# Performance work log

Measured on AMD Instinct MI355X. Metric: run time of the kernel, lower is better.

Reference implementation:

```python
import jax, jax.numpy as jnp
import numpy as np

DROPOUT_RATE = 0.1  # reference runs deterministically (dropout disabled), matching eval-mode math


def setup_inputs() -> dict:
    key = jax.random.key(0)
    k1, k2, k3 = jax.random.split(key, 3)
    BH, S, D = 32, 2048, 64   # batch*heads, seq_len, d_head
    B = 2                      # true batch (mask batch dim)
    q = jax.random.normal(k1, (BH, S, D), dtype=jnp.float32)
    k = jax.random.normal(k2, (BH, S, D), dtype=jnp.float32)
    v = jax.random.normal(k3, (BH, S, D), dtype=jnp.float32)
    mask = jnp.zeros((B, S, S), dtype=jnp.float32)  # additive mask
    return {"q": q, "k": k, "v": v, "mask": mask}


def reference(q, k, v, mask):
    # Scaled dot-product attention with additive mask.
    # q,k,v: [BH, S, D]; mask: [B, S, S], tiled along batch to BH.
    dk = jnp.asarray(k.shape[-1], dtype=jnp.float32)
    scores = jnp.einsum('bqd,bkd->bqk', q, k) / jnp.sqrt(dk)  # [BH, S, S]
    reps = q.shape[0] // mask.shape[0]
    mask_t = jnp.tile(mask, (reps, 1, 1))                     # [BH, S, S]
    attn = jax.nn.softmax(scores + mask_t, axis=-1)
    out = jnp.einsum('bqk,bkd->bqd', attn, v)                 # [BH, S, D]
    # K.dropout omitted: deterministic reference (eval mode / identity)
    return out
```

## Files before the change

kernel.cpp:

```cpp
#include <hip/hip_runtime.h>


constexpr int cBH = 32;
constexpr int cS  = 2048;
constexpr int cD  = 64;
constexpr int cQT = 128;
constexpr int cNP = cS / 128;

typedef __bf16 bf16x8 __attribute__((ext_vector_type(8)));
typedef __bf16 bf16x4 __attribute__((ext_vector_type(4)));
typedef float  f32x4  __attribute__((ext_vector_type(4)));
typedef float  f32x16 __attribute__((ext_vector_type(16)));
typedef unsigned int u32x4 __attribute__((ext_vector_type(4)));

__device__ __forceinline__ unsigned short bfbits(float f) {
    return __builtin_bit_cast(unsigned short, (__bf16)f);
}
__device__ __forceinline__ bf16x4 pack4(f32x4 a) {
    bf16x4 r;
    r[0] = (__bf16)a[0]; r[1] = (__bf16)a[1];
    r[2] = (__bf16)a[2]; r[3] = (__bf16)a[3];
    return r;
}
__device__ __forceinline__ bf16x8 pack8s(f32x4 a, f32x4 b, float s) {
    bf16x8 r;
    r[0] = (__bf16)(a[0]*s); r[1] = (__bf16)(a[1]*s);
    r[2] = (__bf16)(a[2]*s); r[3] = (__bf16)(a[3]*s);
    r[4] = (__bf16)(b[0]*s); r[5] = (__bf16)(b[1]*s);
    r[6] = (__bf16)(b[2]*s); r[7] = (__bf16)(b[3]*s);
    return r;
}
__device__ __forceinline__ int gkey(int d) {
    return (d ^ (d >> 3)) & 7;
}

__global__ __launch_bounds__(256, 2)
void sdpa_flash_kernel(const float* __restrict__ q,
                       const float* __restrict__ k,
                       const float* __restrict__ v,
                       const float* __restrict__ mask,
                       float* __restrict__ out)
{
    __shared__ unsigned short sK[2][64 * 64];
    __shared__ unsigned short sV[2][64 * 64];

    const int tid  = threadIdx.x;
    const int wv   = tid >> 6;
    const int lane = tid & 63;
    const int l31  = lane & 31;
    const int h    = lane >> 5;
    const int swk  = (lane & 7) ^ (((lane >> 3) & 1) << 2);

    const int fid = blockIdx.x;
    const int bh  = (fid & 7) | ((fid >> 7) << 3);
    const int qb  = ((fid >> 3) & 15) * cQT;
    const int mb  = bh & 1;

    const float L2E = 1.4426950408889634f;

    bf16x8 aq[4];
    {
        const float* qp = q + ((size_t)bh * cS + qb + wv * 32 + l31) * cD + h * 8;
#pragma unroll
        for (int dc = 0; dc < 4; ++dc)
            aq[dc] = pack8s(*(const f32x4*)(qp + dc * 16),
                            *(const f32x4*)(qp + dc * 16 + 4), 0.125f * L2E);
    }

    f32x16 acc[2] = {};
    float lsum = 0.f;

    const int sr0 = tid >> 4;
    const int c4  = (tid & 15) << 2;
    const int ka0 = sr0 * 64
        + ((((c4 >> 3) ^ (sr0 & 7) ^ (((sr0 >> 3) & 1) << 2)) << 3))
        + (c4 & 7);
    const float* kg = k + (size_t)bh * cS * cD;
    const float* vg = v + (size_t)bh * cS * cD;
    const float* mq = mask + (size_t)mb * cS * cS
                           + (size_t)(qb + wv * 32 + l31) * cS + h * 4;

    const int g0 = gkey(l31);
    const int g1 = gkey(32 + l31);
    const int vb0 = l31 * 64;
    const int vb1 = (32 + l31) * 64;

#pragma unroll
    for (int t = 0; t < 2; ++t)
#pragma unroll
        for (int j = 0; j < 4; ++j) {
            f32x4 kj = *(const f32x4*)(kg + t * 4096 + j * 1024 + tid * 4);
            f32x4 vj = *(const f32x4*)(vg + t * 4096 + j * 1024 + tid * 4);
            *(bf16x4*)&sK[t][ka0 + j * 1024] = pack4(kj);
#pragma unroll
            for (int i = 0; i < 4; ++i) {
                int d = c4 + i;
                sV[t][d * 64 + ((((j * 2) + (sr0 >> 3)) ^ gkey(d)) << 3) + (sr0 & 7)]
                    = bfbits(vj[i]);
            }
        }

    for (int pt = 0; pt < cNP; ++pt) {
        const int base = pt * 2;
        const bool more = (pt + 1 < cNP);
        const int nb = more ? base + 2 : base;

        f32x4 KPe[4], VPe[4], KPo[4], VPo[4];
#pragma unroll
        for (int j = 0; j < 4; ++j) {
            KPe[j] = *(const f32x4*)(kg + (size_t)nb * 4096 + j * 1024 + tid * 4);
            VPe[j] = *(const f32x4*)(vg + (size_t)nb * 4096 + j * 1024 + tid * 4);
            KPo[j] = *(const f32x4*)(kg + (size_t)(nb + 1) * 4096 + j * 1024 + tid * 4);
            VPo[j] = *(const f32x4*)(vg + (size_t)(nb + 1) * 4096 + j * 1024 + tid * 4);
        }

        __syncthreads();

#pragma unroll
        for (int t = 0; t < 2; ++t) {
            const unsigned short* sKt = sK[t];
            const unsigned short* sVt = sV[t];
#pragma unroll
            for (int gg = 0; gg < 2; ++gg) {
                const float* mrow = mq + (size_t)(base + t) * 64 + gg * 32;
                f32x4 mk[4];
#pragma unroll
                for (int j = 0; j < 4; ++j)
                    mk[j] = *(const f32x4*)(mrow + j * 8);

                const int rb = (gg * 32 + l31) * 64;
                bf16x8 kf[4];
#pragma unroll
                for (int dc = 0; dc < 4; ++dc)
                    kf[dc] = *(const bf16x8*)(&sKt[rb + (((dc * 2 + h) ^ swk) << 3)]);
                f32x16 s = {};
#pragma unroll
                for (int dc = 0; dc < 4; ++dc)
                    s = __builtin_amdgcn_mfma_f32_32x32x16_bf16(kf[dc], aq[dc], s, 0, 0, 0);

                float p[16];
#pragma unroll
                for (int r = 0; r < 16; ++r)
                    p[r] = __builtin_amdgcn_exp2f(fmaf(mk[r >> 2][r & 3], L2E, s[r]));
#pragma unroll
                for (int r = 0; r < 16; ++r)
                    lsum += p[r];

                unsigned int pk[8];
#pragma unroll
                for (int i = 0; i < 8; ++i)
                    pk[i] = (unsigned int)bfbits(p[2 * i])
                          | ((unsigned int)bfbits(p[2 * i + 1]) << 16);
                asm("v_permlane32_swap_b32 %0, %1" : "+v"(pk[0]), "+v"(pk[2]));
                asm("v_permlane32_swap_b32 %0, %1" : "+v"(pk[1]), "+v"(pk[3]));
                asm("v_permlane32_swap_b32 %0, %1" : "+v"(pk[4]), "+v"(pk[6]));
                asm("v_permlane32_swap_b32 %0, %1" : "+v"(pk[5]), "+v"(pk[7]));
                u32x4 ua = {pk[0], pk[1], pk[2], pk[3]};
                u32x4 ub = {pk[4], pk[5], pk[6], pk[7]};
                bf16x8 fA0 = __builtin_bit_cast(bf16x8, ua);
                bf16x8 fA1 = __builtin_bit_cast(bf16x8, ub);

#pragma unroll
                for (int kc = 0; kc < 2; ++kc) {
                    const int kb = gg * 4 + kc * 2 + h;
                    bf16x8 bv0 = *(const bf16x8*)(&sVt[vb0 + ((kb ^ g0) << 3)]);
                    bf16x8 bv1 = *(const bf16x8*)(&sVt[vb1 + ((kb ^ g1) << 3)]);
                    acc[0] = __builtin_amdgcn_mfma_f32_32x32x16_bf16(
                        kc ? fA1 : fA0, bv0, acc[0], 0, 0, 0);
                    acc[1] = __builtin_amdgcn_mfma_f32_32x32x16_bf16(
                        kc ? fA1 : fA0, bv1, acc[1], 0, 0, 0);
                }
            }
        }

        __syncthreads();

        if (more) {
#pragma unroll
            for (int j = 0; j < 4; ++j) {
                *(bf16x4*)&sK[0][ka0 + j * 1024] = pack4(KPe[j]);
                *(bf16x4*)&sK[1][ka0 + j * 1024] = pack4(KPo[j]);
#pragma unroll
                for (int i = 0; i < 4; ++i) {
                    int d = c4 + i;
                    int va = d * 64 + ((((j * 2) + (sr0 >> 3)) ^ gkey(d)) << 3) + (sr0 & 7);
                    sV[0][va] = bfbits(VPe[j][i]);
                    sV[1][va] = bfbits(VPo[j][i]);
                }
            }
        }
    }

    lsum += __shfl_xor(lsum, 32, 64);
#pragma unroll
    for (int r = 0; r < 16; ++r) {
        const int qrow = (r & 3) + 8 * (r >> 2) + 4 * h;
        const float rl = 1.0f / __shfl(lsum, qrow, 64);
        float* op = out + ((size_t)bh * cS + qb + wv * 32 + qrow) * cD + l31;
        op[0]  = acc[0][r] * rl;
        op[32] = acc[1][r] * rl;
    }
}

extern "C" void kernel_launch(void* const* d_in, const int* in_sizes, int n_in,
                              void* d_out, int out_size, void* d_ws, size_t ws_size,
                              hipStream_t stream) {
    const float* q = (const float*)d_in[0];
    const float* k = (const float*)d_in[1];
    const float* v = (const float*)d_in[2];
    const float* m = (const float*)d_in[3];
    float* o = (float*)d_out;
    sdpa_flash_kernel<<<dim3(512), 256, 0, stream>>>(q, k, v, m, o);
}
```

Baseline: 182.5 us.

## Split KV sequence in two across blocks and merge partial sums

Adds a split-K variant: each (bh, q-tile) is processed by two blocks covering halves of the key sequence, writing unnormalized partial outputs and row sums to the workspace. A second merge kernel adds the partials and normalizes. This doubles the grid from 512 to 1024 blocks to fill more CUs on the 256-CU device, at the cost of an extra kernel launch and extra global traffic for the partial output. The original single-pass kernel is kept as a fallback when the workspace is too small.

New measurement: 201.4 us. 1.1x slower.

```diff
diff --git a/kernel.cpp b/kernel.cpp
--- a/kernel.cpp
+++ b/kernel.cpp
@@ -5,7 +5,6 @@
 constexpr int cS  = 2048;
 constexpr int cD  = 64;
 constexpr int cQT = 128;
-constexpr int cNP = cS / 128;
 
 typedef __bf16 bf16x8 __attribute__((ext_vector_type(8)));
 typedef __bf16 bf16x4 __attribute__((ext_vector_type(4)));
@@ -34,12 +33,15 @@
     return (d ^ (d >> 3)) & 7;
 }
 
+template <int NPAIR>
 __global__ __launch_bounds__(256, 2)
-void sdpa_flash_kernel(const float* __restrict__ q,
-                       const float* __restrict__ k,
-                       const float* __restrict__ v,
-                       const float* __restrict__ mask,
-                       float* __restrict__ out)
+void sdpa_part_kernel(const float* __restrict__ q,
+                      const float* __restrict__ k,
+                      const float* __restrict__ v,
+                      const float* __restrict__ mask,
+                      float* __restrict__ out,
+                      float* __restrict__ wsO,
+                      float* __restrict__ wsL)
 {
     __shared__ unsigned short sK[2][64 * 64];
     __shared__ unsigned short sV[2][64 * 64];
@@ -52,9 +54,11 @@
     const int swk  = (lane & 7) ^ (((lane >> 3) & 1) << 2);
 
     const int fid = blockIdx.x;
-    const int bh  = (fid & 7) | ((fid >> 7) << 3);
+    const int bh  = (fid & 7) | (((fid >> 7) & 3) << 3);
     const int qb  = ((fid >> 3) & 15) * cQT;
+    const int kh  = fid >> 9;
     const int mb  = bh & 1;
+    const int koff = kh * (NPAIR * 128);
 
     const float L2E = 1.4426950408889634f;
 
@@ -75,10 +79,10 @@
     const int ka0 = sr0 * 64
         + ((((c4 >> 3) ^ (sr0 & 7) ^ (((sr0 >> 3) & 1) << 2)) << 3))
         + (c4 & 7);
-    const float* kg = k + (size_t)bh * cS * cD;
-    const float* vg = v + (size_t)bh * cS * cD;
+    const float* kg = k + (size_t)bh * cS * cD + (size_t)koff * cD;
+    const float* vg = v + (size_t)bh * cS * cD + (size_t)koff * cD;
     const float* mq = mask + (size_t)mb * cS * cS
-                           + (size_t)(qb + wv * 32 + l31) * cS + h * 4;
+                           + (size_t)(qb + wv * 32 + l31) * cS + koff + h * 4;
 
     const int g0 = gkey(l31);
     const int g1 = gkey(32 + l31);
@@ -100,9 +104,9 @@
             }
         }
 
-    for (int pt = 0; pt < cNP; ++pt) {
+    for (int pt = 0; pt < NPAIR; ++pt) {
         const int base = pt * 2;
-        const bool more = (pt + 1 < cNP);
+        const bool more = (pt + 1 < NPAIR);
         const int nb = more ? base + 2 : base;
 
         f32x4 KPe[4], VPe[4], KPo[4], VPo[4];
@@ -192,6 +196,198 @@
     }
 
     lsum += __shfl_xor(lsum, 32, 64);
+    float* opart = kh ? wsO : out;
+#pragma unroll
+    for (int r = 0; r < 16; ++r) {
+        const int qrow = (r & 3) + 8 * (r >> 2) + 4 * h;
+        float* op = opart + ((size_t)bh * cS + qb + wv * 32 + qrow) * cD + l31;
+        op[0]  = acc[0][r];
+        op[32] = acc[1][r];
+    }
+    if (h == 0)
+        wsL[(size_t)kh * (cBH * cS) + (size_t)bh * cS + qb + wv * 32 + l31] = lsum;
+}
+
+__global__ __launch_bounds__(256)
+void sdpa_merge_kernel(float* __restrict__ out,
+                       const float* __restrict__ wsO,
+                       const float* __restrict__ wsL)
+{
+    const size_t gid = (size_t)blockIdx.x * 256 + threadIdx.x;
+    const size_t e0  = gid * 8;
+    const size_t row = e0 >> 6;
+    const float rl = 1.0f / (wsL[row] + wsL[(size_t)cBH * cS + row]);
+    f32x4 a0 = *(const f32x4*)(out + e0);
+    f32x4 a1 = *(const f32x4*)(out + e0 + 4);
+    f32x4 b0 = *(const f32x4*)(wsO + e0);
+    f32x4 b1 = *(const f32x4*)(wsO + e0 + 4);
+#pragma unroll
+    for (int i = 0; i < 4; ++i) {
+        a0[i] = (a0[i] + b0[i]) * rl;
+        a1[i] = (a1[i] + b1[i]) * rl;
+    }
+    *(f32x4*)(out + e0)     = a0;
+    *(f32x4*)(out + e0 + 4) = a1;
+}
+
+__global__ __launch_bounds__(256, 2)
+void sdpa_flash_kernel(const float* __restrict__ q,
+                       const float* __restrict__ k,
+                       const float* __restrict__ v,
+                       const float* __restrict__ mask,
+                       float* __restrict__ out)
+{
+    __shared__ unsigned short sK[2][64 * 64];
+    __shared__ unsigned short sV[2][64 * 64];
+
+    const int tid  = threadIdx.x;
+    const int wv   = tid >> 6;
+    const int lane = tid & 63;
+    const int l31  = lane & 31;
+    const int h    = lane >> 5;
+    const int swk  = (lane & 7) ^ (((lane >> 3) & 1) << 2);
+
+    const int fid = blockIdx.x;
+    const int bh  = (fid & 7) | ((fid >> 7) << 3);
+    const int qb  = ((fid >> 3) & 15) * cQT;
+    const int mb  = bh & 1;
+
+    const float L2E = 1.4426950408889634f;
+
+    bf16x8 aq[4];
+    {
+        const float* qp = q + ((size_t)bh * cS + qb + wv * 32 + l31) * cD + h * 8;
+#pragma unroll
+        for (int dc = 0; dc < 4; ++dc)
+            aq[dc] = pack8s(*(const f32x4*)(qp + dc * 16),
+                            *(const f32x4*)(qp + dc * 16 + 4), 0.125f * L2E);
+    }
+
+    f32x16 acc[2] = {};
+    float lsum = 0.f;
+
+    const int sr0 = tid >> 4;
+    const int c4  = (tid & 15) << 2;
+    const int ka0 = sr0 * 64
+        + ((((c4 >> 3) ^ (sr0 & 7) ^ (((sr0 >> 3) & 1) << 2)) << 3))
+        + (c4 & 7);
+    const float* kg = k + (size_t)bh * cS * cD;
+    const float* vg = v + (size_t)bh * cS * cD;
+    const float* mq = mask + (size_t)mb * cS * cS
+                           + (size_t)(qb + wv * 32 + l31) * cS + h * 4;
+
+    const int g0 = gkey(l31);
+    const int g1 = gkey(32 + l31);
+    const int vb0 = l31 * 64;
+    const int vb1 = (32 + l31) * 64;
+
+#pragma unroll
+    for (int t = 0; t < 2; ++t)
+#pragma unroll
+        for (int j = 0; j < 4; ++j) {
+            f32x4 kj = *(const f32x4*)(kg + t * 4096 + j * 1024 + tid * 4);
+            f32x4 vj = *(const f32x4*)(vg + t * 4096 + j * 1024 + tid * 4);
+            *(bf16x4*)&sK[t][ka0 + j * 1024] = pack4(kj);
+#pragma unroll
+            for (int i = 0; i < 4; ++i) {
+                int d = c4 + i;
+                sV[t][d * 64 + ((((j * 2) + (sr0 >> 3)) ^ gkey(d)) << 3) + (sr0 & 7)]
+                    = bfbits(vj[i]);
+            }
+        }
+
+    for (int pt = 0; pt < 16; ++pt) {
+        const int base = pt * 2;
+        const bool more = (pt + 1 < 16);
+        const int nb = more ? base + 2 : base;
+
+        f32x4 KPe[4], VPe[4], KPo[4], VPo[4];
+#pragma unroll
+        for (int j = 0; j < 4; ++j) {
+            KPe[j] = *(const f32x4*)(kg + (size_t)nb * 4096 + j * 1024 + tid * 4);
+            VPe[j] = *(const f32x4*)(vg + (size_t)nb * 4096 + j * 1024 + tid * 4);
+            KPo[j] = *(const f32x4*)(kg + (size_t)(nb + 1) * 4096 + j * 1024 + tid * 4);
+            VPo[j] = *(const f32x4*)(vg + (size_t)(nb + 1) * 4096 + j * 1024 + tid * 4);
+        }
+
+        __syncthreads();
+
+#pragma unroll
+        for (int t = 0; t < 2; ++t) {
+            const unsigned short* sKt = sK[t];
+            const unsigned short* sVt = sV[t];
+#pragma unroll
+            for (int gg = 0; gg < 2; ++gg) {
+                const float* mrow = mq + (size_t)(base + t) * 64 + gg * 32;
+                f32x4 mk[4];
+#pragma unroll
+                for (int j = 0; j < 4; ++j)
+                    mk[j] = *(const f32x4*)(mrow + j * 8);
+
+                const int rb = (gg * 32 + l31) * 64;
+                bf16x8 kf[4];
+#pragma unroll
+                for (int dc = 0; dc < 4; ++dc)
+                    kf[dc] = *(const bf16x8*)(&sKt[rb + (((dc * 2 + h) ^ swk) << 3)]);
+                f32x16 s = {};
+#pragma unroll
+                for (int dc = 0; dc < 4; ++dc)
+                    s = __builtin_amdgcn_mfma_f32_32x32x16_bf16(kf[dc], aq[dc], s, 0, 0, 0);
+
+                float p[16];
+#pragma unroll
+                for (int r = 0; r < 16; ++r)
+                    p[r] = __builtin_amdgcn_exp2f(fmaf(mk[r >> 2][r & 3], L2E, s[r]));
+#pragma unroll
+                for (int r = 0; r < 16; ++r)
+                    lsum += p[r];
+
+                unsigned int pk[8];
+#pragma unroll
+                for (int i = 0; i < 8; ++i)
+                    pk[i] = (unsigned int)bfbits(p[2 * i])
+                          | ((unsigned int)bfbits(p[2 * i + 1]) << 16);
+                asm("v_permlane32_swap_b32 %0, %1" : "+v"(pk[0]), "+v"(pk[2]));
+                asm("v_permlane32_swap_b32 %0, %1" : "+v"(pk[1]), "+v"(pk[3]));
+                asm("v_permlane32_swap_b32 %0, %1" : "+v"(pk[4]), "+v"(pk[6]));
+                asm("v_permlane32_swap_b32 %0, %1" : "+v"(pk[5]), "+v"(pk[7]));
+                u32x4 ua = {pk[0], pk[1], pk[2], pk[3]};
+                u32x4 ub = {pk[4], pk[5], pk[6], pk[7]};
+                bf16x8 fA0 = __builtin_bit_cast(bf16x8, ua);
+                bf16x8 fA1 = __builtin_bit_cast(bf16x8, ub);
+
+#pragma unroll
+                for (int kc = 0; kc < 2; ++kc) {
+                    const int kb = gg * 4 + kc * 2 + h;
+                    bf16x8 bv0 = *(const bf16x8*)(&sVt[vb0 + ((kb ^ g0) << 3)]);
+                    bf16x8 bv1 = *(const bf16x8*)(&sVt[vb1 + ((kb ^ g1) << 3)]);
+                    acc[0] = __builtin_amdgcn_mfma_f32_32x32x16_bf16(
+                        kc ? fA1 : fA0, bv0, acc[0], 0, 0, 0);
+                    acc[1] = __builtin_amdgcn_mfma_f32_32x32x16_bf16(
+                        kc ? fA1 : fA0, bv1, acc[1], 0, 0, 0);
+                }
+            }
+        }
+
+        __syncthreads();
+
+        if (more) {
+#pragma unroll
+            for (int j = 0; j < 4; ++j) {
+                *(bf16x4*)&sK[0][ka0 + j * 1024] = pack4(KPe[j]);
+                *(bf16x4*)&sK[1][ka0 + j * 1024] = pack4(KPo[j]);
+#pragma unroll
+                for (int i = 0; i < 4; ++i) {
+                    int d = c4 + i;
+                    int va = d * 64 + ((((j * 2) + (sr0 >> 3)) ^ gkey(d)) << 3) + (sr0 & 7);
+                    sV[0][va] = bfbits(VPe[j][i]);
+                    sV[1][va] = bfbits(VPo[j][i]);
+                }
+            }
+        }
+    }
+
+    lsum += __shfl_xor(lsum, 32, 64);
 #pragma unroll
     for (int r = 0; r < 16; ++r) {
         const int qrow = (r & 3) + 8 * (r >> 2) + 4 * h;
@@ -210,5 +406,17 @@
     const float* v = (const float*)d_in[2];
     const float* m = (const float*)d_in[3];
     float* o = (float*)d_out;
-    sdpa_flash_kernel<<<dim3(512), 256, 0, stream>>>(q, k, v, m, o);
-}
+
+    const size_t nL   = (size_t)2 * cBH * cS;
+    const size_t nO   = (size_t)cBH * cS * cD;
+    const size_t need = (nL + nO) * sizeof(float);
+
+    if (d_ws != nullptr && ws_size >= need) {
+        float* wsL = (float*)d_ws;
+        float* wsO = wsL + nL;
+        sdpa_part_kernel<8><<<dim3(1024), 256, 0, stream>>>(q, k, v, m, o, wsO, wsL);
+        sdpa_merge_kernel<<<dim3((unsigned)(nO / 8 / 256)), 256, 0, stream>>>(o, wsO, wsL);
+    } else {
+        sdpa_flash_kernel<<<dim3(512), 256, 0, stream>>>(q, k, v, m, o);
+    }
+}
```
